# Kernel tuning notes

Hardware: AMD Instinct MI355X
Metric: run time of the kernel (lower is better)

Reference implementation:

```python
import jax, jax.numpy as jnp
import numpy as np
import math

B, TSRC, TTGT, DM, DI, H = 2, 2048, 2048, 1024, 1024, 16
DH = DI // H
LN_EPS = 1e-5


def setup_inputs() -> dict:
    key = jax.random.key(0)
    ks = iter(jax.random.split(key, 40))
    def p(*shape):
        return jax.random.normal(next(ks), shape, jnp.float32) * 0.02
    inp = {
        "enc_out_vecs": jax.random.normal(next(ks), (B, TSRC, DM), jnp.float32),
        "output_vecs": jax.random.normal(next(ks), (B, TTGT, DM), jnp.float32),
    }
    for tag in ("dd", "ed"):
        inp["Wq_" + tag] = p(DM, DI); inp["bq_" + tag] = jnp.zeros((DI,), jnp.float32)
        inp["Wk_" + tag] = p(DM, DI); inp["bk_" + tag] = jnp.zeros((DI,), jnp.float32)
        inp["Wv_" + tag] = p(DM, DI); inp["bv_" + tag] = jnp.zeros((DI,), jnp.float32)
        inp["Wo_" + tag] = p(DI, DM); inp["bo_" + tag] = jnp.zeros((DM,), jnp.float32)
        inp["W1_" + tag] = p(DM, 2 * DM); inp["b1_" + tag] = jnp.zeros((2 * DM,), jnp.float32)
        inp["W2_" + tag] = p(2 * DM, DM); inp["b2_" + tag] = jnp.zeros((DM,), jnp.float32)
        inp["g1_" + tag] = jnp.ones((DM,), jnp.float32); inp["be1_" + tag] = jnp.zeros((DM,), jnp.float32)
        inp["g2_" + tag] = jnp.ones((DM,), jnp.float32); inp["be2_" + tag] = jnp.zeros((DM,), jnp.float32)
    return inp


def _ln(x, g, b):
    m = jnp.mean(x, axis=-1, keepdims=True)
    v = jnp.var(x, axis=-1, keepdims=True)
    return (x - m) * jax.lax.rsqrt(v + LN_EPS) * g + b


def _mha(xq, xkv, Wq, bq, Wk, bk, Wv, bv, causal):
    Bb, Tq, _ = xq.shape
    Tk = xkv.shape[1]
    q = (xq @ Wq + bq).reshape(Bb, Tq, H, DH)
    k = (xkv @ Wk + bk).reshape(Bb, Tk, H, DH)
    v = (xkv @ Wv + bv).reshape(Bb, Tk, H, DH)
    s = jnp.einsum("bqhd,bkhd->bhqk", q, k) / math.sqrt(DH)
    if causal:
        mask = jnp.where(jnp.arange(Tk)[None, :] > jnp.arange(Tq)[:, None], -jnp.inf, 0.0)
        s = s + mask
    w = jax.nn.softmax(s, axis=-1)
    return jnp.einsum("bhqk,bkhd->bqhd", w, v).reshape(Bb, Tq, H * DH)


def reference(enc_out_vecs, output_vecs,
              Wq_dd, bq_dd, Wk_dd, bk_dd, Wv_dd, bv_dd, Wo_dd, bo_dd,
              W1_dd, b1_dd, W2_dd, b2_dd, g1_dd, be1_dd, g2_dd, be2_dd,
              Wq_ed, bq_ed, Wk_ed, bk_ed, Wv_ed, bv_ed, Wo_ed, bo_ed,
              W1_ed, b1_ed, W2_ed, b2_ed, g1_ed, be1_ed, g2_ed, be2_ed):
    # masked self-attention over decoder inputs
    x = output_vecs
    a = _mha(x, x, Wq_dd, bq_dd, Wk_dd, bk_dd, Wv_dd, bv_dd, causal=True)
    x = _ln(a @ Wo_dd + bo_dd + x, g1_dd, be1_dd)
    x = _ln(x + jax.nn.relu(x @ W1_dd + b1_dd) @ W2_dd + b2_dd, g2_dd, be2_dd)
    # cross attention against encoder outputs
    a = _mha(x, enc_out_vecs, Wq_ed, bq_ed, Wk_ed, bk_ed, Wv_ed, bv_ed, causal=False)
    x = _ln(a @ Wo_ed + bo_ed + x, g1_ed, be1_ed)
    x = _ln(jax.nn.relu(x @ W1_ed + b1_ed) @ W2_ed + b2_ed + x, g2_ed, be2_ed)
    return x
```

## Files before the change

kernel.cpp:

```cpp
#include <hip/hip_runtime.h>
#include <stdint.h>

#define DEV __device__ __forceinline__
typedef unsigned short u16;
typedef __attribute__((ext_vector_type(8))) short bf16x8;
typedef __attribute__((ext_vector_type(4))) float f32x4;

#define AS1 __attribute__((address_space(1)))
#define AS3 __attribute__((address_space(3)))
#define WAITVM0 asm volatile("s_waitcnt vmcnt(0)" ::: "memory")
#define QSCALE 0.18033688011112042f

DEV u16 f2bf(float f) {
  union { float f; uint32_t u; } x; x.f = f;
  uint32_t r = x.u + 0x7fffu + ((x.u >> 16) & 1u);
  return (u16)(r >> 16);
}

DEV float bf2f(u16 h) {
  union { uint32_t u; float f; } x; x.u = ((uint32_t)h) << 16;
  return x.f;
}

DEV uint32_t cvt_pk_bf16(float a, float b) {
  uint32_t r;
  asm("v_cvt_pk_bf16_f32 %0, %1, %2" : "=v"(r) : "v"(a), "v"(b));
  return r;
}

__global__ __launch_bounds__(256) void k_cvt2(const float* __restrict__ a, const float* __restrict__ bsrc,
                                              u16* __restrict__ oa, u16* __restrict__ ob, int n4) {
  int i = blockIdx.x * blockDim.x + threadIdx.x;
  const float* s;
  u16* o;
  int k;
  if (i < n4) { s = a; o = oa; k = i; }
  else        { s = bsrc; o = ob; k = i - n4; }
  float4 v = reinterpret_cast<const float4*>(s)[k];
  reinterpret_cast<ushort4*>(o)[k] = make_ushort4(f2bf(v.x), f2bf(v.y), f2bf(v.z), f2bf(v.w));
}

struct WTJob { const float* W; u16* WT; int K, M, msh, start; };
struct WTJobs { WTJob j[12]; };

__global__ void k_wT_all(WTJobs jobs) {
  __shared__ float tile[32][33];
  int b = blockIdx.x;
  int i = 0;
#pragma unroll
  for (int t = 1; t < 12; ++t)
    if (b >= jobs.j[t].start) i = t;
  const WTJob J = jobs.j[i];
  int rel = b - J.start;
  int m0 = (rel & ((1 << J.msh) - 1)) << 5;
  int k0 = (rel >> J.msh) << 5;
  int tx = threadIdx.x, ty = threadIdx.y;
#pragma unroll
  for (int q = 0; q < 4; ++q)
    tile[ty + q * 8][tx] = J.W[(size_t)(k0 + ty + q * 8) * J.M + m0 + tx];
  __syncthreads();
#pragma unroll
  for (int q = 0; q < 4; ++q)
    J.WT[(size_t)(m0 + ty + q * 8) * J.K + k0 + tx] = f2bf(tile[tx][ty + q * 8]);
}

template<int R>
DEV void stage_tile(const u16* __restrict__ g, int strideElems, u16* lds, int tid, int wv) {
#pragma unroll
  for (int t = 0; t < R / 32; ++t) {
    int idx = t * 256 + tid;
    int row = idx >> 3;
    int b = (idx & 7) << 4;
    int sb = b ^ ((row & 7) << 4);
    const char* src = (const char*)g + (size_t)row * strideElems * 2 + sb;
    char* dst = (char*)lds + (size_t)(t * 256 + wv * 64) * 16;
    __builtin_amdgcn_global_load_lds((const AS1 void*)src, (AS3 void*)dst, 16, 0, 0);
  }
}

DEV bf16x8 lds_frag(const u16* lds, int row, int kel) {
  int off = row * 128 + ((kel * 2) ^ ((row & 7) << 4));
  return *(const bf16x8*)((const char*)lds + off);
}

template<int JT, int MODE>
__global__ __launch_bounds__(256) void k_gemm(const u16* __restrict__ A, int lda,
                                              const u16* __restrict__ BT,
                                              const float* __restrict__ bias,
                                              u16* __restrict__ C, int ldc, int K) {
  constexpr int BN = JT * 32;
  __shared__ __align__(16) u16 A_lds[2][128 * 64];
  __shared__ __align__(16) u16 B_lds[2][BN * 64];
  const int tid = threadIdx.x, lane = tid & 63, wv = tid >> 6;
  const int wm = wv >> 1, wn = wv & 1;
  const int nwg = gridDim.x * gridDim.y;
  const int flat = blockIdx.y * gridDim.x + blockIdx.x;
  const int sw = (flat & 7) * (nwg >> 3) + (flat >> 3);
  const int bx = sw % gridDim.x, by = sw / gridDim.x;
  const int bm0 = by * 128, bn0 = bx * BN;
  const int lr = lane & 15, lk = (lane >> 4) * 8, r0 = (lane >> 4) * 4;

  f32x4 acc[4][JT];
#pragma unroll
  for (int i = 0; i < 4; ++i)
#pragma unroll
    for (int j = 0; j < JT; ++j) acc[i][j] = f32x4{0.f, 0.f, 0.f, 0.f};

  stage_tile<128>(A + (size_t)bm0 * lda, lda, A_lds[0], tid, wv);
  stage_tile<BN>(BT + (size_t)bn0 * K, K, B_lds[0], tid, wv);
  WAITVM0;
  __builtin_amdgcn_s_barrier();

  int cur = 0;
  for (int k0 = 0; k0 < K; k0 += 64) {
    if (k0 + 64 < K) {
      stage_tile<128>(A + (size_t)bm0 * lda + k0 + 64, lda, A_lds[cur ^ 1], tid, wv);
      stage_tile<BN>(BT + (size_t)bn0 * K + k0 + 64, K, B_lds[cur ^ 1], tid, wv);
    }
#pragma unroll
    for (int kk = 0; kk < 2; ++kk) {
      bf16x8 af[4], bfr[JT];
#pragma unroll
      for (int i = 0; i < 4; ++i) af[i] = lds_frag(A_lds[cur], wm * 64 + i * 16 + lr, kk * 32 + lk);
#pragma unroll
      for (int j = 0; j < JT; ++j) bfr[j] = lds_frag(B_lds[cur], wn * (JT * 16) + j * 16 + lr, kk * 32 + lk);
#pragma unroll
      for (int i = 0; i < 4; ++i)
#pragma unroll
        for (int j = 0; j < JT; ++j)
          acc[i][j] = __builtin_amdgcn_mfma_f32_16x16x32_bf16(af[i], bfr[j], acc[i][j], 0, 0, 0);
    }
    WAITVM0;
    __builtin_amdgcn_s_barrier();
    cur ^= 1;
  }

#pragma unroll
  for (int j = 0; j < JT; ++j) {
    int col = bn0 + wn * (JT * 16) + j * 16 + lr;
    float bv = bias[col];
#pragma unroll
    for (int i = 0; i < 4; ++i) {
      int rowb = bm0 + wm * 64 + i * 16 + r0;
#pragma unroll
      for (int r = 0; r < 4; ++r) {
        float v = acc[i][j][r] + bv;
        if constexpr (MODE == 2) v = fmaxf(v, 0.f);
        C[(size_t)(rowb + r) * ldc + col] = f2bf(v);
      }
    }
  }
}

__global__ __launch_bounds__(256) void k_qkv(const u16* __restrict__ Aq, const u16* __restrict__ Akv,
                                             const u16* __restrict__ BT,
                                             const float* __restrict__ bq, const float* __restrict__ bk,
                                             const float* __restrict__ bv,
                                             u16* __restrict__ Qb, u16* __restrict__ Kb,
                                             u16* __restrict__ Vt, int K) {
  __shared__ __align__(16) u16 A_lds[2][128 * 64];
  __shared__ __align__(16) u16 B_lds[2][128 * 64];
  const int tid = threadIdx.x, lane = tid & 63, wv = tid >> 6;
  const int wm = wv >> 1, wn = wv & 1;
  const int nwg = gridDim.x * gridDim.y;
  const int flat = blockIdx.y * gridDim.x + blockIdx.x;
  const int sw = (flat & 7) * (nwg >> 3) + (flat >> 3);
  const int bx = sw % gridDim.x, by = sw / gridDim.x;
  const int bm0 = by * 128, bn0 = bx * 128;
  const int seg = bn0 >> 10;
  const u16* A = (seg == 0) ? Aq : Akv;
  const int lr = lane & 15, lk = (lane >> 4) * 8, r0 = (lane >> 4) * 4;

  f32x4 acc[4][4];
#pragma unroll
  for (int i = 0; i < 4; ++i)
#pragma unroll
    for (int j = 0; j < 4; ++j) acc[i][j] = f32x4{0.f, 0.f, 0.f, 0.f};

  stage_tile<128>(A + (size_t)bm0 * K, K, A_lds[0], tid, wv);
  stage_tile<128>(BT + (size_t)bn0 * K, K, B_lds[0], tid, wv);
  WAITVM0;
  __builtin_amdgcn_s_barrier();

  int cur = 0;
  for (int k0 = 0; k0 < K; k0 += 64) {
    if (k0 + 64 < K) {
      stage_tile<128>(A + (size_t)bm0 * K + k0 + 64, K, A_lds[cur ^ 1], tid, wv);
      stage_tile<128>(BT + (size_t)bn0 * K + k0 + 64, K, B_lds[cur ^ 1], tid, wv);
    }
#pragma unroll
    for (int kk = 0; kk < 2; ++kk) {
      bf16x8 af[4], bfr[4];
#pragma unroll
      for (int i = 0; i < 4; ++i) af[i] = lds_frag(A_lds[cur], wm * 64 + i * 16 + lr, kk * 32 + lk);
#pragma unroll
      for (int j = 0; j < 4; ++j) bfr[j] = lds_frag(B_lds[cur], wn * 64 + j * 16 + lr, kk * 32 + lk);
#pragma unroll
      for (int i = 0; i < 4; ++i)
#pragma unroll
        for (int j = 0; j < 4; ++j)
          acc[i][j] = __builtin_amdgcn_mfma_f32_16x16x32_bf16(af[i], bfr[j], acc[i][j], 0, 0, 0);
    }
    WAITVM0;
    __builtin_amdgcn_s_barrier();
    cur ^= 1;
  }

#pragma unroll
  for (int j = 0; j < 4; ++j) {
    int col = bn0 + wn * 64 + j * 16 + lr;
    int cl = col & 1023;
#pragma unroll
    for (int i = 0; i < 4; ++i) {
      int rowb = bm0 + wm * 64 + i * 16 + r0;
      if (seg == 0) {
        float bb = bq[cl];
#pragma unroll
        for (int r = 0; r < 4; ++r)
          Qb[(size_t)(rowb + r) * 1024 + cl] = f2bf((acc[i][j][r] + bb) * QSCALE);
      } else if (seg == 1) {
        float bb = bk[cl];
#pragma unroll
        for (int r = 0; r < 4; ++r)
          Kb[(size_t)(rowb + r) * 1024 + cl] = f2bf(acc[i][j][r] + bb);
      } else {
        float bb = bv[cl];
        int bidx = rowb >> 11, t = rowb & 2047;
        ushort4 o = make_ushort4(f2bf(acc[i][j][0] + bb), f2bf(acc[i][j][1] + bb),
                                 f2bf(acc[i][j][2] + bb), f2bf(acc[i][j][3] + bb));
        *reinterpret_cast<ushort4*>(&Vt[((size_t)bidx * 1024 + cl) * 2048 + t]) = o;
      }
    }
  }
}

__global__ __launch_bounds__(256) void k_ln_b(const u16* __restrict__ Rm, const u16* __restrict__ X,
                                              const float* __restrict__ g, const float* __restrict__ be,
                                              u16* __restrict__ Yb, float* __restrict__ Yf) {
  int row = blockIdx.x;
  size_t base4 = (size_t)row * 256;
  int t = threadIdx.x;
  ushort4 a4 = reinterpret_cast<const ushort4*>(Rm)[base4 + t];
  ushort4 x4 = reinterpret_cast<const ushort4*>(X)[base4 + t];
  float v0 = bf2f(a4.x) + bf2f(x4.x), v1 = bf2f(a4.y) + bf2f(x4.y);
  float v2 = bf2f(a4.z) + bf2f(x4.z), v3 = bf2f(a4.w) + bf2f(x4.w);
  float s = v0 + v1 + v2 + v3;
  float ss = v0 * v0 + v1 * v1 + v2 * v2 + v3 * v3;
#pragma unroll
  for (int m = 1; m < 64; m <<= 1) { s += __shfl_xor(s, m); ss += __shfl_xor(ss, m); }
  __shared__ float red[8];
  int wv = t >> 6;
  if ((t & 63) == 0) { red[wv] = s; red[4 + wv] = ss; }
  __syncthreads();
  s = red[0] + red[1] + red[2] + red[3];
  ss = red[4] + red[5] + red[6] + red[7];
  float mean = s * (1.f / 1024.f);
  float var = ss * (1.f / 1024.f) - mean * mean;
  float rstd = rsqrtf(var + 1e-5f);
  float4 gv = reinterpret_cast<const float4*>(g)[t];
  float4 bv = reinterpret_cast<const float4*>(be)[t];
  float o0 = (v0 - mean) * rstd * gv.x + bv.x;
  float o1 = (v1 - mean) * rstd * gv.y + bv.y;
  float o2 = (v2 - mean) * rstd * gv.z + bv.z;
  float o3 = (v3 - mean) * rstd * gv.w + bv.w;
  if (Yb) {
    ushort4 ob = make_ushort4(f2bf(o0), f2bf(o1), f2bf(o2), f2bf(o3));
    reinterpret_cast<ushort4*>(Yb)[base4 + t] = ob;
  }
  if (Yf)
    reinterpret_cast<float4*>(Yf)[base4 + t] = make_float4(o0, o1, o2, o3);
}

template<bool CAUSAL>
__global__ __launch_bounds__(512) void k_attn(const u16* __restrict__ Q, const u16* __restrict__ Kg,
                                              const u16* __restrict__ Vt, u16* __restrict__ O,
                                              u16* __restrict__ OP0, u16* __restrict__ OP1,
                                              float* __restrict__ L0, float* __restrict__ L1, int T) {
  __shared__ __align__(16) u16 K_lds[3][64 * 64];
  __shared__ __align__(16) u16 V_lds[3][64 * 64];
  __shared__ __align__(16) u16 p_lds[8][16 * 64];
  const int tid = threadIdx.x, lane = tid & 63, wv = tid >> 6;
  const int h = blockIdx.y, b = blockIdx.z;
  const int lq = lane & 15, g = lane >> 4;
  const int swz = (lq & 7) << 4;
  const int fb0 = lq * 128 + ((g * 16) ^ swz);
  const int fb1 = lq * 128 + ((g * 16 + 64) ^ swz);
  const size_t qkbase = ((size_t)b * T) * 1024 + h * 64;
  const size_t vbase = ((size_t)b * 1024 + h * 64) * T;

  int qx, st, en;
  if constexpr (CAUSAL) {
    qx = 15 - (blockIdx.x >> 1);
    const int s = blockIdx.x & 1;
    const int ntf = 2 * qx + 2, half = qx + 1;
    st = s ? half : 0;
    en = s ? ntf : half;
  } else {
    qx = blockIdx.x;
    st = 0;
    en = T >> 6;
  }
  const int qw = qx * 128 + wv * 16;
  const int dtile = qw >> 6;

  bf16x8 aq0, aq1;
  {
    const u16* qp_ = Q + qkbase + (size_t)(qw + lq) * 1024 + g * 8;
    aq0 = *reinterpret_cast<const bf16x8*>(qp_);
    aq1 = *reinterpret_cast<const bf16x8*>(qp_ + 32);
  }

  const int srow = tid >> 3;
  const int ssb = ((tid & 7) << 4) ^ ((srow & 7) << 4);
  const char* ksrc = (const char*)(Kg + qkbase) + (size_t)srow * 2048 + ssb + (size_t)st * 131072;
  const char* vsrc = (const char*)(Vt + vbase) + (size_t)srow * ((size_t)T * 2) + ssb + (size_t)st * 128;
  const uint32_t doff = (uint32_t)(wv << 10);

  auto stage = [&](int buf) {
    __builtin_amdgcn_global_load_lds((const AS1 void*)ksrc, (AS3 void*)((char*)K_lds[buf] + doff), 16, 0, 0);
    __builtin_amdgcn_global_load_lds((const AS1 void*)vsrc, (AS3 void*)((char*)V_lds[buf] + doff), 16, 0, 0);
    ksrc += 131072;
    vsrc += 128;
  };

  f32x4 acc[4];
  float lsum = 0.f;
#pragma unroll
  for (int j = 0; j < 4; ++j) acc[j] = f32x4{0.f, 0.f, 0.f, 0.f};

  char* pw = (char*)p_lds[wv];

  auto qstep = [&](bool domask, int kv0, const char* kb, const char* vb) {
    f32x4 st_[4];
    __builtin_amdgcn_s_setprio(1);
#pragma unroll
    for (int j = 0; j < 4; ++j) {
      bf16x8 bk0 = *reinterpret_cast<const bf16x8*>(kb + fb0 + j * 2048);
      bf16x8 bk1 = *reinterpret_cast<const bf16x8*>(kb + fb1 + j * 2048);
      f32x4 t0 = f32x4{0.f, 0.f, 0.f, 0.f};
      t0 = __builtin_amdgcn_mfma_f32_16x16x32_bf16(bk0, aq0, t0, 0, 0, 0);
      t0 = __builtin_amdgcn_mfma_f32_16x16x32_bf16(bk1, aq1, t0, 0, 0, 0);
      st_[j] = t0;
    }
    __builtin_amdgcn_s_setprio(0);
    uint32_t pk[8];
    if (domask) {
      const int qrow = qw + lq;
#pragma unroll
      for (int j = 0; j < 4; ++j) {
        float p0 = __builtin_exp2f(st_[j][0]);
        float p1 = __builtin_exp2f(st_[j][1]);
        float p2 = __builtin_exp2f(st_[j][2]);
        float p3 = __builtin_exp2f(st_[j][3]);
        int kvb = kv0 + j * 16 + g * 4;
        p0 = (kvb > qrow) ? 0.f : p0;
        p1 = (kvb + 1 > qrow) ? 0.f : p1;
        p2 = (kvb + 2 > qrow) ? 0.f : p2;
        p3 = (kvb + 3 > qrow) ? 0.f : p3;
        lsum += (p0 + p1) + (p2 + p3);
        pk[2 * j] = cvt_pk_bf16(p0, p1);
        pk[2 * j + 1] = cvt_pk_bf16(p2, p3);
      }
    } else {
#pragma unroll
      for (int j = 0; j < 4; ++j) {
        float p0 = __builtin_exp2f(st_[j][0]);
        float p1 = __builtin_exp2f(st_[j][1]);
        float p2 = __builtin_exp2f(st_[j][2]);
        float p3 = __builtin_exp2f(st_[j][3]);
        lsum += (p0 + p1) + (p2 + p3);
        pk[2 * j] = cvt_pk_bf16(p0, p1);
        pk[2 * j + 1] = cvt_pk_bf16(p2, p3);
      }
    }
#pragma unroll
    for (int j = 0; j < 4; ++j)
      *reinterpret_cast<uint2*>(pw + lq * 128 + ((j * 32 + g * 8) ^ swz)) =
          make_uint2(pk[2 * j], pk[2 * j + 1]);
    bf16x8 pf0 = *reinterpret_cast<const bf16x8*>(pw + fb0);
    bf16x8 pf1 = *reinterpret_cast<const bf16x8*>(pw + fb1);
    __builtin_amdgcn_s_setprio(1);
#pragma unroll
    for (int j2 = 0; j2 < 4; ++j2) {
      bf16x8 v0 = *reinterpret_cast<const bf16x8*>(vb + fb0 + j2 * 2048);
      bf16x8 v1 = *reinterpret_cast<const bf16x8*>(vb + fb1 + j2 * 2048);
      acc[j2] = __builtin_amdgcn_mfma_f32_16x16x32_bf16(v0, pf0, acc[j2], 0, 0, 0);
      acc[j2] = __builtin_amdgcn_mfma_f32_16x16x32_bf16(v1, pf1, acc[j2], 0, 0, 0);
    }
    __builtin_amdgcn_s_setprio(0);
  };

  stage(0);
  if (st + 1 < en) {
    stage(1);
    asm volatile("s_waitcnt vmcnt(2)" ::: "memory");
  } else {
    WAITVM0;
  }
  __builtin_amdgcn_s_barrier();

  for (int it = st; it < en; ++it) {
    const int idx = it - st;
    if (it + 2 < en) stage((idx + 2) % 3);
    const char* kb = (const char*)K_lds[idx % 3];
    const char* vb = (const char*)V_lds[idx % 3];
    if (!CAUSAL || it <= dtile)
      qstep(CAUSAL && it == dtile, it << 6, kb, vb);
    if (it + 2 < en) {
      asm volatile("s_waitcnt vmcnt(2)" ::: "memory");
    } else {
      WAITVM0;
    }
    __builtin_amdgcn_s_barrier();
  }

  lsum += __shfl_xor(lsum, 16);
  lsum += __shfl_xor(lsum, 32);
  if constexpr (CAUSAL) {
    u16* OP = (blockIdx.x & 1) ? OP1 : OP0;
    float* Lp = (blockIdx.x & 1) ? L1 : L0;
    const int row = (b * 16 + h) * 2048 + qw + lq;
    u16* pr = OP + (size_t)row * 64;
#pragma unroll
    for (int j2 = 0; j2 < 4; ++j2)
      *reinterpret_cast<uint2*>(pr + j2 * 16 + g * 4) =
          make_uint2(cvt_pk_bf16(acc[j2][0], acc[j2][1]), cvt_pk_bf16(acc[j2][2], acc[j2][3]));
    if (g == 0) Lp[row] = lsum;
  } else {
    float inv = 1.f / lsum;
    size_t rb = qkbase + (size_t)(qw + lq) * 1024;
#pragma unroll
    for (int j2 = 0; j2 < 4; ++j2) {
      ushort4 o = make_ushort4(f2bf(acc[j2][0] * inv), f2bf(acc[j2][1] * inv),
                               f2bf(acc[j2][2] * inv), f2bf(acc[j2][3] * inv));
      *reinterpret_cast<ushort4*>(&O[rb + j2 * 16 + g * 4]) = o;
    }
  }
}

__global__ __launch_bounds__(256) void k_amrg(const u16* __restrict__ P0, const u16* __restrict__ P1,
                                              const float* __restrict__ L0, const float* __restrict__ L1,
                                              u16* __restrict__ Ab) {
  int i = blockIdx.x * 256 + threadIdx.x;
  int row = i >> 4, d4 = (i & 15) << 2;
  ushort4 a4 = *reinterpret_cast<const ushort4*>(&P0[(size_t)row * 64 + d4]);
  ushort4 c4 = *reinterpret_cast<const ushort4*>(&P1[(size_t)row * 64 + d4]);
  float inv = 1.f / (L0[row] + L1[row]);
  int bh = row >> 11, q = row & 2047, bb = bh >> 4, hh = bh & 15;
  size_t dst = ((size_t)(bb * 2048 + q)) * 1024 + hh * 64 + d4;
  ushort4 o = make_ushort4(f2bf((bf2f(a4.x) + bf2f(c4.x)) * inv), f2bf((bf2f(a4.y) + bf2f(c4.y)) * inv),
                           f2bf((bf2f(a4.z) + bf2f(c4.z)) * inv), f2bf((bf2f(a4.w) + bf2f(c4.w)) * inv));
  *reinterpret_cast<ushort4*>(&Ab[dst]) = o;
}

extern "C" void kernel_launch(void* const* d_in, const int* in_sizes, int n_in,
                              void* d_out, int out_size, void* d_ws, size_t ws_size,
                              hipStream_t stream) {
  const int T = 2048;
  const float* enc = (const float*)d_in[0];
  const float* outv = (const float*)d_in[1];
  auto F = [&](int i) { return (const float*)d_in[i]; };

  size_t off = 0;
  auto alloc = [&](size_t bytes) {
    void* p = (char*)d_ws + off;
    off += (bytes + 255) & ~(size_t)255;
    return p;
  };

  const int tdK[12] = {1024, 1024, 1024, 1024, 1024, 2048, 1024, 1024, 1024, 1024, 1024, 2048};
  const int tdM[12] = {1024, 1024, 1024, 1024, 2048, 1024, 1024, 1024, 1024, 1024, 2048, 1024};
  const int tdIdx[12] = {2, 4, 6, 8, 10, 12, 18, 20, 22, 24, 26, 28};
  u16* WT_[12];
  for (int i = 0; i < 12; ++i) WT_[i] = (u16*)alloc((size_t)tdK[i] * tdM[i] * 2);

  u16* Xb0 = (u16*)alloc(4096ull * 1024 * 2);
  u16* Eb = (u16*)alloc(4096ull * 1024 * 2);
  u16* Qb = (u16*)alloc(4096ull * 1024 * 2);
  u16* Kb = (u16*)alloc(4096ull * 1024 * 2);
  u16* Vt = (u16*)alloc(4096ull * 1024 * 2);
  u16* Ab = (u16*)alloc(4096ull * 1024 * 2);
  u16* Hb = (u16*)alloc(4096ull * 2048 * 2);
  u16* Rm = (u16*)alloc(4096ull * 1024 * 2);
  u16* X1b = (u16*)alloc(4096ull * 1024 * 2);
  u16* X2b = (u16*)alloc(4096ull * 1024 * 2);
  u16* X3b = (u16*)alloc(4096ull * 1024 * 2);
  u16* OP0 = (u16*)alloc(4096ull * 1024 * 2);
  u16* OP1 = (u16*)alloc(4096ull * 1024 * 2);
  float* Lsum = (float*)alloc(2ull * 65536 * 4);

  k_cvt2<<<8192, 256, 0, stream>>>(outv, enc, Xb0, Eb, 4096 * 1024 / 4);

  WTJobs jobs;
  int start = 0;
  for (int i = 0; i < 12; ++i) {
    int msh = (tdM[i] == 2048) ? 6 : 5;
    jobs.j[i] = {F(tdIdx[i]), WT_[i], tdK[i], tdM[i], msh, start};
    start += (tdM[i] >> 5) * (tdK[i] >> 5);
  }
  k_wT_all<<<start, dim3(32, 8), 0, stream>>>(jobs);

  float* L0 = Lsum;
  float* L1 = Lsum + 65536;

  dim3 gq(24, 32);
  dim3 g1k(16, 32);
  dim3 g2k(16, 32);
  dim3 gac(32, 16, 2);
  dim3 gan(16, 16, 2);

  k_qkv<<<gq, 256, 0, stream>>>(Xb0, Xb0, WT_[0], F(3), F(5), F(7), Qb, Kb, Vt, 1024);
  k_attn<true><<<gac, 512, 0, stream>>>(Qb, Kb, Vt, Ab, OP0, OP1, L0, L1, T);
  k_amrg<<<4096, 256, 0, stream>>>(OP0, OP1, L0, L1, Ab);
  k_gemm<2, 1><<<g1k, 256, 0, stream>>>(Ab, 1024, WT_[3], F(9), Rm, 1024, 1024);
  k_ln_b<<<4096, 256, 0, stream>>>(Rm, Xb0, F(14), F(15), X1b, nullptr);
  k_gemm<4, 2><<<g2k, 256, 0, stream>>>(X1b, 1024, WT_[4], F(11), Hb, 2048, 1024);
  k_gemm<2, 1><<<g1k, 256, 0, stream>>>(Hb, 2048, WT_[5], F(13), Rm, 1024, 2048);
  k_ln_b<<<4096, 256, 0, stream>>>(Rm, X1b, F(16), F(17), X2b, nullptr);

  k_qkv<<<gq, 256, 0, stream>>>(X2b, Eb, WT_[6], F(19), F(21), F(23), Qb, Kb, Vt, 1024);
  k_attn<false><<<gan, 512, 0, stream>>>(Qb, Kb, Vt, Ab, OP0, OP1, L0, L1, T);
  k_gemm<2, 1><<<g1k, 256, 0, stream>>>(Ab, 1024, WT_[9], F(25), Rm, 1024, 1024);
  k_ln_b<<<4096, 256, 0, stream>>>(Rm, X2b, F(30), F(31), X3b, nullptr);
  k_gemm<4, 2><<<g2k, 256, 0, stream>>>(X3b, 1024, WT_[10], F(27), Hb, 2048, 1024);
  k_gemm<2, 1><<<g1k, 256, 0, stream>>>(Hb, 2048, WT_[11], F(29), Rm, 1024, 2048);
  k_ln_b<<<4096, 256, 0, stream>>>(Rm, X3b, F(32), F(33), nullptr, (float*)d_out);
}
```

Baseline: 423.3 us.

## Drop causal split-KV attention with merge kernel and fuse init kernels

Causal attention now runs one block per 128-query tile over the full KV range, in reverse order so the longest tiles start first. This replaces the two-way split plus the separate merge kernel that combined partials through global memory. The input bf16 conversion and weight transpose kernels are also merged into one launch. The change removes one launch and the partial-result traffic, but leaves 512 blocks of uneven length for causal attention, which may hurt load balance.

After: 412.6 us. 2.5% less time.

```diff
diff --git a/kernel.cpp b/kernel.cpp
--- a/kernel.cpp
+++ b/kernel.cpp
@@ -28,24 +28,26 @@
   return r;
 }
 
-__global__ __launch_bounds__(256) void k_cvt2(const float* __restrict__ a, const float* __restrict__ bsrc,
-                                              u16* __restrict__ oa, u16* __restrict__ ob, int n4) {
-  int i = blockIdx.x * blockDim.x + threadIdx.x;
-  const float* s;
-  u16* o;
-  int k;
-  if (i < n4) { s = a; o = oa; k = i; }
-  else        { s = bsrc; o = ob; k = i - n4; }
-  float4 v = reinterpret_cast<const float4*>(s)[k];
-  reinterpret_cast<ushort4*>(o)[k] = make_ushort4(f2bf(v.x), f2bf(v.y), f2bf(v.z), f2bf(v.w));
-}
-
 struct WTJob { const float* W; u16* WT; int K, M, msh, start; };
 struct WTJobs { WTJob j[12]; };
 
-__global__ void k_wT_all(WTJobs jobs) {
+__global__ __launch_bounds__(256) void k_init(WTJobs jobs, int wtBlocks,
+                                              const float* __restrict__ a, const float* __restrict__ bsrc,
+                                              u16* __restrict__ oa, u16* __restrict__ ob, int n4) {
   __shared__ float tile[32][33];
   int b = blockIdx.x;
+  int tid = threadIdx.x;
+  if (b >= wtBlocks) {
+    int i = (b - wtBlocks) * 256 + tid;
+    const float* s;
+    u16* o;
+    int k;
+    if (i < n4) { s = a; o = oa; k = i; }
+    else        { s = bsrc; o = ob; k = i - n4; }
+    float4 v = reinterpret_cast<const float4*>(s)[k];
+    reinterpret_cast<ushort4*>(o)[k] = make_ushort4(f2bf(v.x), f2bf(v.y), f2bf(v.z), f2bf(v.w));
+    return;
+  }
   int i = 0;
 #pragma unroll
   for (int t = 1; t < 12; ++t)
@@ -54,7 +56,7 @@
   int rel = b - J.start;
   int m0 = (rel & ((1 << J.msh) - 1)) << 5;
   int k0 = (rel >> J.msh) << 5;
-  int tx = threadIdx.x, ty = threadIdx.y;
+  int tx = tid & 31, ty = tid >> 5;
 #pragma unroll
   for (int q = 0; q < 4; ++q)
     tile[ty + q * 8][tx] = J.W[(size_t)(k0 + ty + q * 8) * J.M + m0 + tx];
@@ -273,9 +275,7 @@
 
 template<bool CAUSAL>
 __global__ __launch_bounds__(512) void k_attn(const u16* __restrict__ Q, const u16* __restrict__ Kg,
-                                              const u16* __restrict__ Vt, u16* __restrict__ O,
-                                              u16* __restrict__ OP0, u16* __restrict__ OP1,
-                                              float* __restrict__ L0, float* __restrict__ L1, int T) {
+                                              const u16* __restrict__ Vt, u16* __restrict__ O, int T) {
   __shared__ __align__(16) u16 K_lds[3][64 * 64];
   __shared__ __align__(16) u16 V_lds[3][64 * 64];
   __shared__ __align__(16) u16 p_lds[8][16 * 64];
@@ -288,18 +288,8 @@
   const size_t qkbase = ((size_t)b * T) * 1024 + h * 64;
   const size_t vbase = ((size_t)b * 1024 + h * 64) * T;
 
-  int qx, st, en;
-  if constexpr (CAUSAL) {
-    qx = 15 - (blockIdx.x >> 1);
-    const int s = blockIdx.x & 1;
-    const int ntf = 2 * qx + 2, half = qx + 1;
-    st = s ? half : 0;
-    en = s ? ntf : half;
-  } else {
-    qx = blockIdx.x;
-    st = 0;
-    en = T >> 6;
-  }
+  const int qx = CAUSAL ? (gridDim.x - 1 - blockIdx.x) : blockIdx.x;
+  const int en = CAUSAL ? (2 * qx + 2) : (T >> 6);
   const int qw = qx * 128 + wv * 16;
   const int dtile = qw >> 6;
 
@@ -312,8 +302,8 @@
 
   const int srow = tid >> 3;
   const int ssb = ((tid & 7) << 4) ^ ((srow & 7) << 4);
-  const char* ksrc = (const char*)(Kg + qkbase) + (size_t)srow * 2048 + ssb + (size_t)st * 131072;
-  const char* vsrc = (const char*)(Vt + vbase) + (size_t)srow * ((size_t)T * 2) + ssb + (size_t)st * 128;
+  const char* ksrc = (const char*)(Kg + qkbase) + (size_t)srow * 2048 + ssb;
+  const char* vsrc = (const char*)(Vt + vbase) + (size_t)srow * ((size_t)T * 2) + ssb;
   const uint32_t doff = (uint32_t)(wv << 10);
 
   auto stage = [&](int buf) {
@@ -391,7 +381,7 @@
   };
 
   stage(0);
-  if (st + 1 < en) {
+  if (en > 1) {
     stage(1);
     asm volatile("s_waitcnt vmcnt(2)" ::: "memory");
   } else {
@@ -399,11 +389,10 @@
   }
   __builtin_amdgcn_s_barrier();
 
-  for (int it = st; it < en; ++it) {
-    const int idx = it - st;
-    if (it + 2 < en) stage((idx + 2) % 3);
-    const char* kb = (const char*)K_lds[idx % 3];
-    const char* vb = (const char*)V_lds[idx % 3];
+  for (int it = 0; it < en; ++it) {
+    if (it + 2 < en) stage((it + 2) % 3);
+    const char* kb = (const char*)K_lds[it % 3];
+    const char* vb = (const char*)V_lds[it % 3];
     if (!CAUSAL || it <= dtile)
       qstep(CAUSAL && it == dtile, it << 6, kb, vb);
     if (it + 2 < en) {
@@ -416,41 +405,14 @@
 
   lsum += __shfl_xor(lsum, 16);
   lsum += __shfl_xor(lsum, 32);
-  if constexpr (CAUSAL) {
-    u16* OP = (blockIdx.x & 1) ? OP1 : OP0;
-    float* Lp = (blockIdx.x & 1) ? L1 : L0;
-    const int row = (b * 16 + h) * 2048 + qw + lq;
-    u16* pr = OP + (size_t)row * 64;
-#pragma unroll
-    for (int j2 = 0; j2 < 4; ++j2)
-      *reinterpret_cast<uint2*>(pr + j2 * 16 + g * 4) =
-          make_uint2(cvt_pk_bf16(acc[j2][0], acc[j2][1]), cvt_pk_bf16(acc[j2][2], acc[j2][3]));
-    if (g == 0) Lp[row] = lsum;
-  } else {
-    float inv = 1.f / lsum;
-    size_t rb = qkbase + (size_t)(qw + lq) * 1024;
-#pragma unroll
-    for (int j2 = 0; j2 < 4; ++j2) {
-      ushort4 o = make_ushort4(f2bf(acc[j2][0] * inv), f2bf(acc[j2][1] * inv),
-                               f2bf(acc[j2][2] * inv), f2bf(acc[j2][3] * inv));
-      *reinterpret_cast<ushort4*>(&O[rb + j2 * 16 + g * 4]) = o;
-    }
-  }
-}
-
-__global__ __launch_bounds__(256) void k_amrg(const u16* __restrict__ P0, const u16* __restrict__ P1,
-                                              const float* __restrict__ L0, const float* __restrict__ L1,
-                                              u16* __restrict__ Ab) {
-  int i = blockIdx.x * 256 + threadIdx.x;
-  int row = i >> 4, d4 = (i & 15) << 2;
-  ushort4 a4 = *reinterpret_cast<const ushort4*>(&P0[(size_t)row * 64 + d4]);
-  ushort4 c4 = *reinterpret_cast<const ushort4*>(&P1[(size_t)row * 64 + d4]);
-  float inv = 1.f / (L0[row] + L1[row]);
-  int bh = row >> 11, q = row & 2047, bb = bh >> 4, hh = bh & 15;
-  size_t dst = ((size_t)(bb * 2048 + q)) * 1024 + hh * 64 + d4;
-  ushort4 o = make_ushort4(f2bf((bf2f(a4.x) + bf2f(c4.x)) * inv), f2bf((bf2f(a4.y) + bf2f(c4.y)) * inv),
-                           f2bf((bf2f(a4.z) + bf2f(c4.z)) * inv), f2bf((bf2f(a4.w) + bf2f(c4.w)) * inv));
-  *reinterpret_cast<ushort4*>(&Ab[dst]) = o;
+  float inv = 1.f / lsum;
+  size_t rb = qkbase + (size_t)(qw + lq) * 1024;
+#pragma unroll
+  for (int j2 = 0; j2 < 4; ++j2) {
+    ushort4 o = make_ushort4(f2bf(acc[j2][0] * inv), f2bf(acc[j2][1] * inv),
+                             f2bf(acc[j2][2] * inv), f2bf(acc[j2][3] * inv));
+    *reinterpret_cast<ushort4*>(&O[rb + j2 * 16 + g * 4]) = o;
+  }
 }
 
 extern "C" void kernel_launch(void* const* d_in, const int* in_sizes, int n_in,
@@ -485,11 +447,6 @@
   u16* X1b = (u16*)alloc(4096ull * 1024 * 2);
   u16* X2b = (u16*)alloc(4096ull * 1024 * 2);
   u16* X3b = (u16*)alloc(4096ull * 1024 * 2);
-  u16* OP0 = (u16*)alloc(4096ull * 1024 * 2);
-  u16* OP1 = (u16*)alloc(4096ull * 1024 * 2);
-  float* Lsum = (float*)alloc(2ull * 65536 * 4);
-
-  k_cvt2<<<8192, 256, 0, stream>>>(outv, enc, Xb0, Eb, 4096 * 1024 / 4);
 
   WTJobs jobs;
   int start = 0;
@@ -498,20 +455,16 @@
     jobs.j[i] = {F(tdIdx[i]), WT_[i], tdK[i], tdM[i], msh, start};
     start += (tdM[i] >> 5) * (tdK[i] >> 5);
   }
-  k_wT_all<<<start, dim3(32, 8), 0, stream>>>(jobs);
-
-  float* L0 = Lsum;
-  float* L1 = Lsum + 65536;
+  const int n4 = 4096 * 1024 / 4;
+  k_init<<<start + 8192, 256, 0, stream>>>(jobs, start, outv, enc, Xb0, Eb, n4);
 
   dim3 gq(24, 32);
   dim3 g1k(16, 32);
   dim3 g2k(16, 32);
-  dim3 gac(32, 16, 2);
-  dim3 gan(16, 16, 2);
+  dim3 ga(16, 16, 2);
 
   k_qkv<<<gq, 256, 0, stream>>>(Xb0, Xb0, WT_[0], F(3), F(5), F(7), Qb, Kb, Vt, 1024);
-  k_attn<true><<<gac, 512, 0, stream>>>(Qb, Kb, Vt, Ab, OP0, OP1, L0, L1, T);
-  k_amrg<<<4096, 256, 0, stream>>>(OP0, OP1, L0, L1, Ab);
+  k_attn<true><<<ga, 512, 0, stream>>>(Qb, Kb, Vt, Ab, T);
   k_gemm<2, 1><<<g1k, 256, 0, stream>>>(Ab, 1024, WT_[3], F(9), Rm, 1024, 1024);
   k_ln_b<<<4096, 256, 0, stream>>>(Rm, Xb0, F(14), F(15), X1b, nullptr);
   k_gemm<4, 2><<<g2k, 256, 0, stream>>>(X1b, 1024, WT_[4], F(11), Hb, 2048, 1024);
@@ -519,7 +472,7 @@
   k_ln_b<<<4096, 256, 0, stream>>>(Rm, X1b, F(16), F(17), X2b, nullptr);
 
   k_qkv<<<gq, 256, 0, stream>>>(X2b, Eb, WT_[6], F(19), F(21), F(23), Qb, Kb, Vt, 1024);
-  k_attn<false><<<gan, 512, 0, stream>>>(Qb, Kb, Vt, Ab, OP0, OP1, L0, L1, T);
+  k_attn<false><<<ga, 512, 0, stream>>>(Qb, Kb, Vt, Ab, T);
   k_gemm<2, 1><<<g1k, 256, 0, stream>>>(Ab, 1024, WT_[9], F(25), Rm, 1024, 1024);
   k_ln_b<<<4096, 256, 0, stream>>>(Rm, X2b, F(30), F(31), X3b, nullptr);
   k_gemm<4, 2><<<g2k, 256, 0, stream>>>(X3b, 1024, WT_[10], F(27), Hb, 2048, 1024);
```
